# Performance work log

Measured on AMD Instinct MI355X. Metric: run time of the kernel, lower is better.

The kernel has to match this reference:

```python
import jax, jax.numpy as jnp
import numpy as np

N = 40000      # nodes (adj.size(0))
ISIZE = 64     # feature dim
K = 24         # kept kNN neighbors per node after d_cut mask
E = N * K      # learner candidate edges
E_ADJ = N * K  # GCN adjacency edges
OMEGA = 0.9
GAMMA = 2.0
D_CUT = 1.5


def setup_inputs() -> dict:
    key = jax.random.key(0)
    k = jax.random.split(key, 8)
    features = jax.random.normal(k[0], (N, ISIZE), jnp.float32)
    sc = 1.0 / np.sqrt(ISIZE)
    W1 = jax.random.normal(k[1], (ISIZE, ISIZE), jnp.float32) * sc
    b1 = jnp.zeros((ISIZE,), jnp.float32)
    W2 = jax.random.normal(k[2], (ISIZE, ISIZE), jnp.float32) * sc
    b2 = jnp.zeros((ISIZE,), jnp.float32)
    adj_row = jax.random.randint(k[3], (E_ADJ,), 0, N, dtype=jnp.int32)
    adj_col = jax.random.randint(k[4], (E_ADJ,), 0, N, dtype=jnp.int32)
    # kNN-style candidate edges: K neighbors per node, no self loops
    i_idx = jnp.repeat(jnp.arange(N, dtype=jnp.int32), K)
    j_idx = (i_idx + jax.random.randint(k[5], (E,), 1, N, dtype=jnp.int32)) % N
    # precomputed distance prior: s_d = 1/exp(gamma*(d/d_cut)^2)
    dist = jax.random.uniform(k[6], (E,), jnp.float32, 0.1, 2.0)
    s_d = jnp.exp(-GAMMA * (dist / D_CUT) ** 2)
    return {"features": features, "W1": W1, "b1": b1, "W2": W2, "b2": b2,
            "s_d": s_d, "adj_row": adj_row, "adj_col": adj_col,
            "i_idx": i_idx, "j_idx": j_idx}


def _gcn(x, W, b, row, col):
    """PyG GCNConv: symmetric norm with self loops, aggregate src=row into dst=col."""
    xw = x @ W
    deg = 1.0 + jax.ops.segment_sum(jnp.ones((row.shape[0],), jnp.float32), col,
                                    num_segments=N)
    dinv = jax.lax.rsqrt(deg)
    msg = (dinv[row] * dinv[col])[:, None] * xw[row]            # [E_ADJ, ISIZE]
    out = jax.ops.segment_sum(msg, col, num_segments=N)
    return out + (dinv * dinv)[:, None] * xw + b                # self-loop + bias


def reference(features, W1, b1, W2, b2, s_d, adj_row, adj_col, i_idx, j_idx):
    # GCN stack (nlayers=2), ReLU between layers
    h = jax.nn.relu(_gcn(features, W1, b1, adj_row, adj_col))
    h = _gcn(h, W2, b2, adj_row, adj_col)
    # F.normalize(h, p=2, dim=-1)
    h = h / jnp.maximum(jnp.linalg.norm(h, axis=-1, keepdims=True), 1e-12)
    # per-edge cosine scores, clamped at 0, blended with distance prior
    s_val = jnp.sum(h[i_idx] * h[j_idx], axis=-1)               # [E]
    s_val = jax.nn.relu(s_val)
    s_val = OMEGA * s_val + (1.0 - OMEGA) * s_d
    # SparseTensor.to_symmetric(reduce='mean'): average with reverse edge if present
    keys = i_idx * N + j_idx                                    # fits int32 (N=4e4)
    rkeys = j_idx * N + i_idx
    order = jnp.argsort(keys)
    sk = keys[order]
    pos = jnp.clip(jnp.searchsorted(sk, rkeys), 0, E - 1)
    found = sk[pos] == rkeys
    rev = order[pos]
    v_sym = jnp.where(found, 0.5 * (s_val + s_val[rev]), s_val)
    # symmetric COO: original edges + reverse copies (zeroed where reverse existed)
    rows_s = jnp.concatenate([i_idx, j_idx])                    # [2E]
    cols_s = jnp.concatenate([j_idx, i_idx])
    vals_s = jnp.concatenate([v_sym, jnp.where(found, 0.0, v_sym)])
    # normalize_adj_symm: D^{-1/2} S D^{-1/2}
    deg = jax.ops.segment_sum(vals_s, rows_s, num_segments=N)
    dinv = jnp.where(deg > 0, jax.lax.rsqrt(jnp.maximum(deg, 1e-12)), 0.0)
    vals_norm = dinv[rows_s] * vals_s * dinv[cols_s]
    return vals_norm, vals_s
```

## Files before the change

### kernel.cpp

```cpp
#include <hip/hip_runtime.h>

#define N_NODES 40000
#define ISIZE   64
#define KNN     24
#define NE      (N_NODES * KNN)
#define OMEGA   0.9f
#define CAP     64
#define NBUCK   80
#define BCAP    16384
#define JBCAP   16384
#define EPT     8

__device__ __forceinline__ float bf2f(unsigned short s) {
    return __uint_as_float(((unsigned)s) << 16);
}
__device__ __forceinline__ unsigned short f2bf(float f) {
    unsigned u = __float_as_uint(f);
    u += 0x7fffu + ((u >> 16) & 1u);
    return (unsigned short)(u >> 16);
}
__device__ __forceinline__ float bflo(unsigned u) { return __uint_as_float(u << 16); }
__device__ __forceinline__ float bfhi(unsigned u) { return __uint_as_float(u & 0xffff0000u); }
__device__ __forceinline__ unsigned pack2(float lo, float hi) {
    return (unsigned)f2bf(lo) | ((unsigned)f2bf(hi) << 16);
}

__global__ void k_mega1(const float* __restrict__ X, const float* __restrict__ W,
                        unsigned short* __restrict__ Y0, unsigned short* __restrict__ Y1,
                        const int* __restrict__ row, const int* __restrict__ col,
                        const int* __restrict__ j_idx,
                        int* __restrict__ bcnt, unsigned* __restrict__ bbuf,
                        unsigned* __restrict__ ovf2, int* __restrict__ ovf2_cnt,
                        int* __restrict__ jbcnt, unsigned* __restrict__ jbbuf,
                        unsigned* __restrict__ jovf, int* __restrict__ jovf_cnt,
                        unsigned char* __restrict__ revb) {
    __shared__ float sW[64 * 64];
    __shared__ float sX[32 * 64];
    const int GB  = N_NODES / 32;
    const int NBA = (NE + 256 * EPT - 1) / (256 * EPT);
    int bx = blockIdx.x;
    int tid = threadIdx.x;
    if (bx < GB) {
        int row0 = bx * 32;
        for (int t = tid; t < 1024; t += 256)
            ((float4*)sW)[t] = ((const float4*)W)[t];
        for (int t = tid; t < 512; t += 256)
            ((float4*)sX)[t] = ((const float4*)(X + row0 * 64))[t];
        __syncthreads();
        int cc = tid & 63;
        int rl = tid >> 6;
        for (int r = rl; r < 32; r += 4) {
            float acc = 0.0f;
#pragma unroll
            for (int kk = 0; kk < 64; kk++) acc += sX[r * 64 + kk] * sW[kk * 64 + cc];
            if (cc < 32) Y0[(row0 + r) * 32 + cc]      = f2bf(acc);
            else         Y1[(row0 + r) * 32 + cc - 32] = f2bf(acc);
        }
    } else if (bx < GB + 2 * NBA) {
        int* lcnt  = (int*)sW;
        int* lbase = lcnt + NBUCK;
        int blk = bx - GB;
        bool adj = blk < NBA;
        if (!adj) blk -= NBA;
        for (int b = tid; b < NBUCK; b += 256) lcnt[b] = 0;
        __syncthreads();
        int e0 = blk * (256 * EPT);
        int myslot[EPT]; int myb[EPT]; unsigned myp[EPT];
        for (int k = 0; k < EPT; k++) {
            int e = e0 + k * 256 + tid;
            if (e < NE) {
                int b; unsigned p;
                if (adj) { int r = row[e], c = col[e]; b = c >> 9; p = ((unsigned)r << 16) | (unsigned)c; }
                else     { int j = j_idx[e];           b = j >> 9; p = ((unsigned)(j & 511) << 20) | (unsigned)e; }
                myb[k] = b; myp[k] = p;
                myslot[k] = atomicAdd(&lcnt[b], 1);
            } else myb[k] = -1;
        }
        __syncthreads();
        int* gcnt = adj ? bcnt : jbcnt;
        for (int b = tid; b < NBUCK; b += 256)
            lbase[b] = (lcnt[b] > 0) ? atomicAdd(&gcnt[b], lcnt[b]) : 0;
        __syncthreads();
        unsigned* gbuf = adj ? bbuf : jbbuf;
        unsigned* govf = adj ? ovf2 : jovf;
        int* gocnt = adj ? ovf2_cnt : jovf_cnt;
        for (int k = 0; k < EPT; k++) {
            if (myb[k] < 0) continue;
            int pos = lbase[myb[k]] + myslot[k];
            if (pos < BCAP) gbuf[myb[k] * BCAP + pos] = myp[k];
            else { int p = atomicAdd(gocnt, 1); govf[p] = myp[k]; }
        }
    } else {
        int e = (bx - GB - 2 * NBA) * 256 + tid;
        int i = e / KNN;
        int j = j_idx[e];
        const uint4* jj4 = (const uint4*)(j_idx + j * KNN);
        int rt = 255;
#pragma unroll
        for (int k = 5; k >= 0; k--) {
            uint4 u = jj4[k];
            if ((int)u.w == i) rt = 4 * k + 3;
            if ((int)u.z == i) rt = 4 * k + 2;
            if ((int)u.y == i) rt = 4 * k + 1;
            if ((int)u.x == i) rt = 4 * k + 0;
        }
        revb[e] = (unsigned char)rt;
    }
}

__global__ void k_scatter3(const unsigned* __restrict__ bbuf, const int* __restrict__ bcnt,
                           int* __restrict__ cnt, unsigned short* __restrict__ ebuf,
                           unsigned* __restrict__ ovf, int* __restrict__ ovf_cnt,
                           const unsigned* __restrict__ ovf2, const int* __restrict__ ovf2_cnt) {
    __shared__ int lcnt2[512];
    int b = blockIdx.x;
    int tid = threadIdx.x;
    if (tid < 512) lcnt2[tid] = 0;
    __syncthreads();
    int n = min(bcnt[b], BCAP);
    for (int idx = tid; idx < n; idx += 1024) {
        unsigned p = bbuf[b * BCAP + idx];
        int c = (int)(p & 0xffffu), r = (int)(p >> 16);
        int slot = atomicAdd(&lcnt2[c & 511], 1);
        if (slot < CAP) ebuf[c * CAP + slot] = (unsigned short)r;
        else { int q = atomicAdd(ovf_cnt, 1); ovf[q] = p; }
    }
    int m = ovf2_cnt[0];
    for (int idx = tid; idx < m; idx += 1024) {
        unsigned p = ovf2[idx];
        int c = (int)(p & 0xffffu), r = (int)(p >> 16);
        if ((c >> 9) != b) continue;
        int slot = atomicAdd(&lcnt2[c & 511], 1);
        if (slot < CAP) ebuf[c * CAP + slot] = (unsigned short)r;
        else { int q = atomicAdd(ovf_cnt, 1); ovf[q] = p; }
    }
    __syncthreads();
    if (tid < 512) {
        int node = b * 512 + tid;
        if (node < N_NODES) cnt[node] = lcnt2[tid];
    }
}

__global__ void k_gemm2(const unsigned short* __restrict__ X, const float* __restrict__ W,
                        unsigned short* __restrict__ Y0, unsigned short* __restrict__ Y1) {
    __shared__ float sW[64 * 64];
    __shared__ float sX[32 * 64];
    int row0 = blockIdx.x * 32;
    for (int t = threadIdx.x; t < 1024; t += 256)
        ((float4*)sW)[t] = ((const float4*)W)[t];
    for (int t = threadIdx.x; t < 512; t += 256) {
        uint2 u = ((const uint2*)(X + row0 * 64))[t];
        ((float4*)sX)[t] = make_float4(bflo(u.x), bfhi(u.x), bflo(u.y), bfhi(u.y));
    }
    __syncthreads();
    int col = threadIdx.x & 63;
    int rl  = threadIdx.x >> 6;
    for (int r = rl; r < 32; r += 4) {
        float acc = 0.0f;
#pragma unroll
        for (int kk = 0; kk < 64; kk++) acc += sX[r * 64 + kk] * sW[kk * 64 + col];
        if (col < 32) Y0[(row0 + r) * 32 + col]      = f2bf(acc);
        else          Y1[(row0 + r) * 32 + col - 32] = f2bf(acc);
    }
}

template<bool RELU, bool NORM>
__global__ void k_aggf4(const uint4* __restrict__ X0q, const uint4* __restrict__ X1q,
                        uint4* __restrict__ outFq,
                        uint4* __restrict__ O0q, uint4* __restrict__ O1q,
                        const int* __restrict__ cnt,
                        const unsigned short* __restrict__ ebuf, const float* __restrict__ bias,
                        const unsigned* __restrict__ ovf, const int* __restrict__ ovf_cnt) {
    int w = (blockIdx.x * 256 + threadIdx.x) >> 6;
    int lane = threadIdx.x & 63;
    int half = lane >> 5, sl = lane & 31;
    int n = w * 2 + half;
    if (n >= N_NODES) return;
    int deg = cnt[n];
    int bucketed = min(deg, CAP);
    int nb0 = min(bucketed, 32);
    int nb1 = bucketed - nb0;

    int   r0v = 0, r1v = 0;
    float d0v = 0.0f, d1v = 0.0f;
    if (sl < nb0) { r0v = (int)ebuf[n * CAP + sl];      d0v = rsqrtf(1.0f + (float)cnt[r0v]); }
    if (sl < nb1) { r1v = (int)ebuf[n * CAP + 32 + sl]; d1v = rsqrtf(1.0f + (float)cnt[r1v]); }

    int g = sl >> 2;
    int f = sl & 3;

    float a[16];
#pragma unroll
    for (int k = 0; k < 16; k++) a[k] = 0.f;

    int np0 = (nb0 + 7) >> 3;
    int np1 = (nb1 + 7) >> 3;

#pragma unroll 4
    for (int d = 0; d < np0; d++) {
        int   q = 8 * d + g;
        int   r = __shfl(r0v, q, 32);
        float c = __shfl(d0v, q, 32);
        uint4 u0 = X0q[r * 4 + f];
        uint4 u1 = X1q[r * 4 + f];
        a[0]  += c * bflo(u0.x); a[1]  += c * bfhi(u0.x);
        a[2]  += c * bflo(u0.y); a[3]  += c * bfhi(u0.y);
        a[4]  += c * bflo(u0.z); a[5]  += c * bfhi(u0.z);
        a[6]  += c * bflo(u0.w); a[7]  += c * bfhi(u0.w);
        a[8]  += c * bflo(u1.x); a[9]  += c * bfhi(u1.x);
        a[10] += c * bflo(u1.y); a[11] += c * bfhi(u1.y);
        a[12] += c * bflo(u1.z); a[13] += c * bfhi(u1.z);
        a[14] += c * bflo(u1.w); a[15] += c * bfhi(u1.w);
    }
#pragma unroll 4
    for (int d = 0; d < np1; d++) {
        int   q = 8 * d + g;
        int   r = __shfl(r1v, q, 32);
        float c = __shfl(d1v, q, 32);
        uint4 u0 = X0q[r * 4 + f];
        uint4 u1 = X1q[r * 4 + f];
        a[0]  += c * bflo(u0.x); a[1]  += c * bfhi(u0.x);
        a[2]  += c * bflo(u0.y); a[3]  += c * bfhi(u0.y);
        a[4]  += c * bflo(u0.z); a[5]  += c * bfhi(u0.z);
        a[6]  += c * bflo(u0.w); a[7]  += c * bfhi(u0.w);
        a[8]  += c * bflo(u1.x); a[9]  += c * bfhi(u1.x);
        a[10] += c * bflo(u1.y); a[11] += c * bfhi(u1.y);
        a[12] += c * bflo(u1.z); a[13] += c * bfhi(u1.z);
        a[14] += c * bflo(u1.w); a[15] += c * bfhi(u1.w);
    }

    if (deg > CAP) {
        int m = ovf_cnt[0];
        for (int k2 = 0; k2 < m; k2++) {
            unsigned p = ovf[k2];
            if ((int)(p & 0xffffu) == n && g == 0) {
                int r = (int)(p >> 16);
                float c = rsqrtf(1.0f + (float)cnt[r]);
                uint4 u0 = X0q[r * 4 + f], u1 = X1q[r * 4 + f];
                a[0]  += c * bflo(u0.x); a[1]  += c * bfhi(u0.x);
                a[2]  += c * bflo(u0.y); a[3]  += c * bfhi(u0.y);
                a[4]  += c * bflo(u0.z); a[5]  += c * bfhi(u0.z);
                a[6]  += c * bflo(u0.w); a[7]  += c * bfhi(u0.w);
                a[8]  += c * bflo(u1.x); a[9]  += c * bfhi(u1.x);
                a[10] += c * bflo(u1.y); a[11] += c * bfhi(u1.y);
                a[12] += c * bflo(u1.z); a[13] += c * bfhi(u1.z);
                a[14] += c * bflo(u1.w); a[15] += c * bfhi(u1.w);
            }
        }
    }

#pragma unroll
    for (int k = 0; k < 16; k++) {
        a[k] += __shfl_xor(a[k], 4, 32);
        a[k] += __shfl_xor(a[k], 8, 32);
        a[k] += __shfl_xor(a[k], 16, 32);
    }

    float di = rsqrtf(1.0f + (float)deg);
    float dd = di * di;
    uint4 s0 = X0q[n * 4 + f], s1 = X1q[n * 4 + f];
    float4 bA0 = ((const float4*)bias)[2 * f];
    float4 bA1 = ((const float4*)bias)[2 * f + 1];
    float4 bB0 = ((const float4*)(bias + 32))[2 * f];
    float4 bB1 = ((const float4*)(bias + 32))[2 * f + 1];
    float v[16];
    v[0]  = di * a[0]  + dd * bflo(s0.x) + bA0.x;
    v[1]  = di * a[1]  + dd * bfhi(s0.x) + bA0.y;
    v[2]  = di * a[2]  + dd * bflo(s0.y) + bA0.z;
    v[3]  = di * a[3]  + dd * bfhi(s0.y) + bA0.w;
    v[4]  = di * a[4]  + dd * bflo(s0.z) + bA1.x;
    v[5]  = di * a[5]  + dd * bfhi(s0.z) + bA1.y;
    v[6]  = di * a[6]  + dd * bflo(s0.w) + bA1.z;
    v[7]  = di * a[7]  + dd * bfhi(s0.w) + bA1.w;
    v[8]  = di * a[8]  + dd * bflo(s1.x) + bB0.x;
    v[9]  = di * a[9]  + dd * bfhi(s1.x) + bB0.y;
    v[10] = di * a[10] + dd * bflo(s1.y) + bB0.z;
    v[11] = di * a[11] + dd * bfhi(s1.y) + bB0.w;
    v[12] = di * a[12] + dd * bflo(s1.z) + bB1.x;
    v[13] = di * a[13] + dd * bfhi(s1.z) + bB1.y;
    v[14] = di * a[14] + dd * bflo(s1.w) + bB1.z;
    v[15] = di * a[15] + dd * bfhi(s1.w) + bB1.w;
    if (RELU) {
#pragma unroll
        for (int k = 0; k < 16; k++) v[k] = fmaxf(v[k], 0.f);
    }
    if (NORM) {
        float s = 0.f;
#pragma unroll
        for (int k = 0; k < 16; k++) s += v[k] * v[k];
        s += __shfl_xor(s, 1, 32);
        s += __shfl_xor(s, 2, 32);
        float inv = 1.0f / fmaxf(sqrtf(s), 1e-12f);
#pragma unroll
        for (int k = 0; k < 16; k++) v[k] *= inv;
        if (g == 0) {
            O0q[n * 4 + f] = make_uint4(pack2(v[0], v[1]),  pack2(v[2], v[3]),
                                        pack2(v[4], v[5]),  pack2(v[6], v[7]));
            O1q[n * 4 + f] = make_uint4(pack2(v[8], v[9]),  pack2(v[10], v[11]),
                                        pack2(v[12], v[13]), pack2(v[14], v[15]));
        }
    } else {
        if (g == 0) {
            outFq[n * 8 + f]     = make_uint4(pack2(v[0], v[1]),  pack2(v[2], v[3]),
                                              pack2(v[4], v[5]),  pack2(v[6], v[7]));
            outFq[n * 8 + 4 + f] = make_uint4(pack2(v[8], v[9]),  pack2(v[10], v[11]),
                                              pack2(v[12], v[13]), pack2(v[14], v[15]));
        }
    }
}

__global__ void k_dotsym(const uint4* __restrict__ H0q, const uint4* __restrict__ H1q,
                         const float* __restrict__ s_d, const int* __restrict__ j_idx,
                         const unsigned char* __restrict__ revb,
                         float* __restrict__ outS) {
    int t = blockIdx.x * 256 + threadIdx.x;
    int e = t >> 3;
    int q = t & 7;
    int g = q >> 2, f = q & 3;
    int i = e / KNN;
    int j = j_idx[e];
    int node = g ? j : i;
    uint4 u0 = H0q[node * 4 + f];
    uint4 u1 = H1q[node * 4 + f];
    uint4 p0, p1;
    p0.x = __shfl_xor(u0.x, 4); p0.y = __shfl_xor(u0.y, 4);
    p0.z = __shfl_xor(u0.z, 4); p0.w = __shfl_xor(u0.w, 4);
    p1.x = __shfl_xor(u1.x, 4); p1.y = __shfl_xor(u1.y, 4);
    p1.z = __shfl_xor(u1.z, 4); p1.w = __shfl_xor(u1.w, 4);
    float s = bflo(u0.x) * bflo(p0.x) + bfhi(u0.x) * bfhi(p0.x)
            + bflo(u0.y) * bflo(p0.y) + bfhi(u0.y) * bfhi(p0.y)
            + bflo(u0.z) * bflo(p0.z) + bfhi(u0.z) * bfhi(p0.z)
            + bflo(u0.w) * bflo(p0.w) + bfhi(u0.w) * bfhi(p0.w)
            + bflo(u1.x) * bflo(p1.x) + bfhi(u1.x) * bfhi(p1.x)
            + bflo(u1.y) * bflo(p1.y) + bfhi(u1.y) * bfhi(p1.y)
            + bflo(u1.z) * bflo(p1.z) + bfhi(u1.z) * bfhi(p1.z)
            + bflo(u1.w) * bflo(p1.w) + bfhi(u1.w) * bfhi(p1.w);
    s += __shfl_xor(s, 1);
    s += __shfl_xor(s, 2);
    if (q == 0) {
        float base = OMEGA * fmaxf(s, 0.0f);
        int rt = revb[e];
        float vv, v2;
        if (rt != 255) {
            int rev = j * KNN + rt;
            vv = base + 0.5f * (1.0f - OMEGA) * (s_d[e] + s_d[rev]);
            v2 = 0.0f;
        } else {
            vv = base + (1.0f - OMEGA) * s_d[e];
            v2 = vv;
        }
        outS[e] = vv;
        outS[NE + e] = v2;
    }
}

__global__ void k_jagg(const unsigned* __restrict__ jbbuf, const int* __restrict__ jbcnt,
                       const float* __restrict__ outS, float* __restrict__ dinv2,
                       const unsigned* __restrict__ jovf, const int* __restrict__ jovf_cnt,
                       const int* __restrict__ j_idx) {
    __shared__ float ld[512];
    int b = blockIdx.x;
    int tid = threadIdx.x;
    if (tid < 512) ld[tid] = 0.0f;
    __syncthreads();
    const float* outSv2 = outS + NE;
    int n = min(jbcnt[b], JBCAP);
    for (int idx = tid; idx < n; idx += 1024) {
        unsigned p = jbbuf[b * JBCAP + idx];
        atomicAdd(&ld[p >> 20], outSv2[p & 0xFFFFFu]);
    }
    int m = jovf_cnt[0];
    for (int t2 = tid; t2 < m; t2 += 1024) {
        int e = (int)(jovf[t2] & 0xFFFFFu);
        int j = j_idx[e];
        if ((j >> 9) == b) atomicAdd(&ld[j & 511], outSv2[e]);
    }
    __syncthreads();
    if (tid < 512) {
        int node = b * 512 + tid;
        if (node < N_NODES) {
            float d = ld[tid];
            const float* pp = outS + node * KNN;
#pragma unroll
            for (int qq = 0; qq < KNN; qq++) d += pp[qq];
            dinv2[node] = (d > 0.0f) ? rsqrtf(fmaxf(d, 1e-12f)) : 0.0f;
        }
    }
}

__global__ void k_norm(const float* __restrict__ outS, const float* __restrict__ dinv2,
                       const int* __restrict__ j_idx, float* __restrict__ out) {
    int t = blockIdx.x * 256 + threadIdx.x;
    int r, c;
    if (t < NE) { r = t / KNN; c = j_idx[t]; }
    else        { int e = t - NE; r = j_idx[e]; c = e / KNN; }
    out[t] = dinv2[r] * outS[t] * dinv2[c];
}

extern "C" void kernel_launch(void* const* d_in, const int* in_sizes, int n_in,
                              void* d_out, int out_size, void* d_ws, size_t ws_size,
                              hipStream_t stream) {
    const float* features = (const float*)d_in[0];
    const float* W1       = (const float*)d_in[1];
    const float* b1       = (const float*)d_in[2];
    const float* W2       = (const float*)d_in[3];
    const float* b2       = (const float*)d_in[4];
    const float* s_d      = (const float*)d_in[5];
    const int*   adj_row  = (const int*)d_in[6];
    const int*   adj_col  = (const int*)d_in[7];
    const int*   j_idx    = (const int*)d_in[9];
    float* out = (float*)d_out;

    const int N64 = N_NODES * 64;
    const int N32 = N_NODES * 32;
    int*   cnt     = (int*)d_ws;
    int*   ovfcnts = cnt + N_NODES;
    int*   bcnt    = ovfcnts + 16;
    int*   jbcnt   = bcnt + NBUCK;
    float* dinv2   = (float*)(jbcnt + NBUCK);
    unsigned short* A0  = (unsigned short*)(dinv2 + N_NODES);
    unsigned short* A1  = A0 + N32;
    unsigned short* B16 = A1 + N32;
    unsigned short* H0  = B16 + N64;
    unsigned short* H1  = H0 + N32;
    unsigned short* ebuf = H1 + N32;
    unsigned* ovf    = (unsigned*)(ebuf + N_NODES * CAP);
    unsigned char* revb = (unsigned char*)(ovf + NE);
    unsigned* bbuf   = (unsigned*)(revb + NE);
    unsigned* jbbuf  = bbuf + NBUCK * BCAP;
    unsigned* ovf2   = jbbuf + NBUCK * JBCAP;
    unsigned* jovf   = ovf2 + NE;

    size_t zero_bytes = (size_t)(N_NODES + 16 + 2 * NBUCK) * 4;
    hipMemsetAsync(cnt, 0, zero_bytes, stream);

    const int GB = N_NODES / 32;
    const int NBA = (NE + 256 * EPT - 1) / (256 * EPT);
    const int RB = NE / 256;
    k_mega1<<<GB + 2 * NBA + RB, 256, 0, stream>>>(
        features, W1, A0, A1, adj_row, adj_col, j_idx,
        bcnt, bbuf, ovf2, ovfcnts + 4, jbcnt, jbbuf, jovf, ovfcnts + 8, revb);

    k_scatter3<<<NBUCK, 1024, 0, stream>>>(bbuf, bcnt, cnt, ebuf,
                                           ovf, ovfcnts, ovf2, ovfcnts + 4);

    k_aggf4<true, false><<<(N_NODES / 2 * 64 + 255) / 256, 256, 0, stream>>>(
        (const uint4*)A0, (const uint4*)A1, (uint4*)B16, nullptr, nullptr,
        cnt, ebuf, b1, ovf, ovfcnts);

    k_gemm2<<<N_NODES / 32, 256, 0, stream>>>(B16, W2, A0, A1);
    k_aggf4<false, true><<<(N_NODES / 2 * 64 + 255) / 256, 256, 0, stream>>>(
        (const uint4*)A0, (const uint4*)A1, nullptr, (uint4*)H0, (uint4*)H1,
        cnt, ebuf, b2, ovf, ovfcnts);

    float* outS = out + 2 * NE;
    k_dotsym<<<NE * 8 / 256, 256, 0, stream>>>(
        (const uint4*)H0, (const uint4*)H1, s_d, j_idx, revb, outS);

    k_jagg<<<NBUCK, 1024, 0, stream>>>(jbbuf, jbcnt, outS, dinv2, jovf, ovfcnts + 8, j_idx);
    k_norm<<<2 * NE / 256, 256, 0, stream>>>(outS, dinv2, j_idx, out);
}
```

Measured before the change: 252.0 us.

## Fuse layer-1 aggregation with second GEMM and halve dot-product threads per edge

Merges the first GCN aggregation (with ReLU and bias) and the following 64x64 GEMM into one 1024-thread kernel. The aggregated rows stay in shared memory and are multiplied by W2 there, which removes the bf16 intermediate round-trip through global memory and one kernel launch. The edge dot-product kernel now uses 4 threads per edge, each loading both endpoints directly instead of exchanging halves through shuffles, so it launches half as many threads. In exchange the fused kernel needs a block-wide barrier and large blocks, with launch bounds forcing one block per SM, which may reduce latency hiding for the gather-heavy aggregation.

Result: faster. 236.4 us (-6.2%).

```diff
diff --git a/kernel.cpp b/kernel.cpp
--- a/kernel.cpp
+++ b/kernel.cpp
@@ -141,41 +141,23 @@
     }
 }
 
-__global__ void k_gemm2(const unsigned short* __restrict__ X, const float* __restrict__ W,
-                        unsigned short* __restrict__ Y0, unsigned short* __restrict__ Y1) {
+__global__ void __launch_bounds__(1024, 1)
+k_aggemm1(const uint4* __restrict__ X0q, const uint4* __restrict__ X1q,
+          const float* __restrict__ W2,
+          unsigned short* __restrict__ C0, unsigned short* __restrict__ C1,
+          const int* __restrict__ cnt,
+          const unsigned short* __restrict__ ebuf, const float* __restrict__ bias,
+          const unsigned* __restrict__ ovf, const int* __restrict__ ovf_cnt) {
     __shared__ float sW[64 * 64];
-    __shared__ float sX[32 * 64];
-    int row0 = blockIdx.x * 32;
-    for (int t = threadIdx.x; t < 1024; t += 256)
-        ((float4*)sW)[t] = ((const float4*)W)[t];
-    for (int t = threadIdx.x; t < 512; t += 256) {
-        uint2 u = ((const uint2*)(X + row0 * 64))[t];
-        ((float4*)sX)[t] = make_float4(bflo(u.x), bfhi(u.x), bflo(u.y), bfhi(u.y));
-    }
-    __syncthreads();
-    int col = threadIdx.x & 63;
-    int rl  = threadIdx.x >> 6;
-    for (int r = rl; r < 32; r += 4) {
-        float acc = 0.0f;
-#pragma unroll
-        for (int kk = 0; kk < 64; kk++) acc += sX[r * 64 + kk] * sW[kk * 64 + col];
-        if (col < 32) Y0[(row0 + r) * 32 + col]      = f2bf(acc);
-        else          Y1[(row0 + r) * 32 + col - 32] = f2bf(acc);
-    }
-}
-
-template<bool RELU, bool NORM>
-__global__ void k_aggf4(const uint4* __restrict__ X0q, const uint4* __restrict__ X1q,
-                        uint4* __restrict__ outFq,
-                        uint4* __restrict__ O0q, uint4* __restrict__ O1q,
-                        const int* __restrict__ cnt,
-                        const unsigned short* __restrict__ ebuf, const float* __restrict__ bias,
-                        const unsigned* __restrict__ ovf, const int* __restrict__ ovf_cnt) {
-    int w = (blockIdx.x * 256 + threadIdx.x) >> 6;
-    int lane = threadIdx.x & 63;
+    __shared__ float sB[32 * 64];
+    int tid  = threadIdx.x;
+    int lane = tid & 63;
     int half = lane >> 5, sl = lane & 31;
-    int n = w * 2 + half;
-    if (n >= N_NODES) return;
+    int nl = (tid >> 6) * 2 + half;
+    int n  = blockIdx.x * 32 + nl;
+
+    ((float4*)sW)[tid] = ((const float4*)W2)[tid];
+
     int deg = cnt[n];
     int bucketed = min(deg, CAP);
     int nb0 = min(bucketed, 32);
@@ -192,7 +174,6 @@
     float a[16];
 #pragma unroll
     for (int k = 0; k < 16; k++) a[k] = 0.f;
-
     int np0 = (nb0 + 7) >> 3;
     int np1 = (nb1 + 7) >> 3;
 
@@ -228,7 +209,6 @@
         a[12] += c * bflo(u1.z); a[13] += c * bfhi(u1.z);
         a[14] += c * bflo(u1.w); a[15] += c * bfhi(u1.w);
     }
-
     if (deg > CAP) {
         int m = ovf_cnt[0];
         for (int k2 = 0; k2 < m; k2++) {
@@ -248,7 +228,142 @@
             }
         }
     }
-
+#pragma unroll
+    for (int k = 0; k < 16; k++) {
+        a[k] += __shfl_xor(a[k], 4, 32);
+        a[k] += __shfl_xor(a[k], 8, 32);
+        a[k] += __shfl_xor(a[k], 16, 32);
+    }
+
+    float di = rsqrtf(1.0f + (float)deg);
+    float dd = di * di;
+    uint4 s0 = X0q[n * 4 + f], s1 = X1q[n * 4 + f];
+    float4 bA0 = ((const float4*)bias)[2 * f];
+    float4 bA1 = ((const float4*)bias)[2 * f + 1];
+    float4 bB0 = ((const float4*)(bias + 32))[2 * f];
+    float4 bB1 = ((const float4*)(bias + 32))[2 * f + 1];
+    if (g == 0) {
+        float* dst = sB + nl * 64 + 8 * f;
+        dst[0] = fmaxf(di * a[0]  + dd * bflo(s0.x) + bA0.x, 0.f);
+        dst[1] = fmaxf(di * a[1]  + dd * bfhi(s0.x) + bA0.y, 0.f);
+        dst[2] = fmaxf(di * a[2]  + dd * bflo(s0.y) + bA0.z, 0.f);
+        dst[3] = fmaxf(di * a[3]  + dd * bfhi(s0.y) + bA0.w, 0.f);
+        dst[4] = fmaxf(di * a[4]  + dd * bflo(s0.z) + bA1.x, 0.f);
+        dst[5] = fmaxf(di * a[5]  + dd * bfhi(s0.z) + bA1.y, 0.f);
+        dst[6] = fmaxf(di * a[6]  + dd * bflo(s0.w) + bA1.z, 0.f);
+        dst[7] = fmaxf(di * a[7]  + dd * bfhi(s0.w) + bA1.w, 0.f);
+        float* dst2 = dst + 32;
+        dst2[0] = fmaxf(di * a[8]  + dd * bflo(s1.x) + bB0.x, 0.f);
+        dst2[1] = fmaxf(di * a[9]  + dd * bfhi(s1.x) + bB0.y, 0.f);
+        dst2[2] = fmaxf(di * a[10] + dd * bflo(s1.y) + bB0.z, 0.f);
+        dst2[3] = fmaxf(di * a[11] + dd * bfhi(s1.y) + bB0.w, 0.f);
+        dst2[4] = fmaxf(di * a[12] + dd * bflo(s1.z) + bB1.x, 0.f);
+        dst2[5] = fmaxf(di * a[13] + dd * bfhi(s1.z) + bB1.y, 0.f);
+        dst2[6] = fmaxf(di * a[14] + dd * bflo(s1.w) + bB1.z, 0.f);
+        dst2[7] = fmaxf(di * a[15] + dd * bfhi(s1.w) + bB1.w, 0.f);
+    }
+    __syncthreads();
+
+    int col = tid & 63;
+    int r0  = tid >> 6;
+    float acc0 = 0.f, acc1 = 0.f;
+#pragma unroll
+    for (int kk = 0; kk < 64; kk++) {
+        float wv = sW[kk * 64 + col];
+        acc0 += sB[r0 * 64 + kk] * wv;
+        acc1 += sB[(r0 + 16) * 64 + kk] * wv;
+    }
+    int na = blockIdx.x * 32 + r0;
+    int nb = na + 16;
+    if (col < 32) {
+        C0[na * 32 + col] = f2bf(acc0);
+        C0[nb * 32 + col] = f2bf(acc1);
+    } else {
+        C1[na * 32 + col - 32] = f2bf(acc0);
+        C1[nb * 32 + col - 32] = f2bf(acc1);
+    }
+}
+
+__global__ void k_aggf4(const uint4* __restrict__ X0q, const uint4* __restrict__ X1q,
+                        uint4* __restrict__ O0q, uint4* __restrict__ O1q,
+                        const int* __restrict__ cnt,
+                        const unsigned short* __restrict__ ebuf, const float* __restrict__ bias,
+                        const unsigned* __restrict__ ovf, const int* __restrict__ ovf_cnt) {
+    int w = (blockIdx.x * 256 + threadIdx.x) >> 6;
+    int lane = threadIdx.x & 63;
+    int half = lane >> 5, sl = lane & 31;
+    int n = w * 2 + half;
+    if (n >= N_NODES) return;
+    int deg = cnt[n];
+    int bucketed = min(deg, CAP);
+    int nb0 = min(bucketed, 32);
+    int nb1 = bucketed - nb0;
+
+    int   r0v = 0, r1v = 0;
+    float d0v = 0.0f, d1v = 0.0f;
+    if (sl < nb0) { r0v = (int)ebuf[n * CAP + sl];      d0v = rsqrtf(1.0f + (float)cnt[r0v]); }
+    if (sl < nb1) { r1v = (int)ebuf[n * CAP + 32 + sl]; d1v = rsqrtf(1.0f + (float)cnt[r1v]); }
+
+    int g = sl >> 2;
+    int f = sl & 3;
+
+    float a[16];
+#pragma unroll
+    for (int k = 0; k < 16; k++) a[k] = 0.f;
+    int np0 = (nb0 + 7) >> 3;
+    int np1 = (nb1 + 7) >> 3;
+
+#pragma unroll 4
+    for (int d = 0; d < np0; d++) {
+        int   q = 8 * d + g;
+        int   r = __shfl(r0v, q, 32);
+        float c = __shfl(d0v, q, 32);
+        uint4 u0 = X0q[r * 4 + f];
+        uint4 u1 = X1q[r * 4 + f];
+        a[0]  += c * bflo(u0.x); a[1]  += c * bfhi(u0.x);
+        a[2]  += c * bflo(u0.y); a[3]  += c * bfhi(u0.y);
+        a[4]  += c * bflo(u0.z); a[5]  += c * bfhi(u0.z);
+        a[6]  += c * bflo(u0.w); a[7]  += c * bfhi(u0.w);
+        a[8]  += c * bflo(u1.x); a[9]  += c * bfhi(u1.x);
+        a[10] += c * bflo(u1.y); a[11] += c * bfhi(u1.y);
+        a[12] += c * bflo(u1.z); a[13] += c * bfhi(u1.z);
+        a[14] += c * bflo(u1.w); a[15] += c * bfhi(u1.w);
+    }
+#pragma unroll 4
+    for (int d = 0; d < np1; d++) {
+        int   q = 8 * d + g;
+        int   r = __shfl(r1v, q, 32);
+        float c = __shfl(d1v, q, 32);
+        uint4 u0 = X0q[r * 4 + f];
+        uint4 u1 = X1q[r * 4 + f];
+        a[0]  += c * bflo(u0.x); a[1]  += c * bfhi(u0.x);
+        a[2]  += c * bflo(u0.y); a[3]  += c * bfhi(u0.y);
+        a[4]  += c * bflo(u0.z); a[5]  += c * bfhi(u0.z);
+        a[6]  += c * bflo(u0.w); a[7]  += c * bfhi(u0.w);
+        a[8]  += c * bflo(u1.x); a[9]  += c * bfhi(u1.x);
+        a[10] += c * bflo(u1.y); a[11] += c * bfhi(u1.y);
+        a[12] += c * bflo(u1.z); a[13] += c * bfhi(u1.z);
+        a[14] += c * bflo(u1.w); a[15] += c * bfhi(u1.w);
+    }
+    if (deg > CAP) {
+        int m = ovf_cnt[0];
+        for (int k2 = 0; k2 < m; k2++) {
+            unsigned p = ovf[k2];
+            if ((int)(p & 0xffffu) == n && g == 0) {
+                int r = (int)(p >> 16);
+                float c = rsqrtf(1.0f + (float)cnt[r]);
+                uint4 u0 = X0q[r * 4 + f], u1 = X1q[r * 4 + f];
+                a[0]  += c * bflo(u0.x); a[1]  += c * bfhi(u0.x);
+                a[2]  += c * bflo(u0.y); a[3]  += c * bfhi(u0.y);
+                a[4]  += c * bflo(u0.z); a[5]  += c * bfhi(u0.z);
+                a[6]  += c * bflo(u0.w); a[7]  += c * bfhi(u0.w);
+                a[8]  += c * bflo(u1.x); a[9]  += c * bfhi(u1.x);
+                a[10] += c * bflo(u1.y); a[11] += c * bfhi(u1.y);
+                a[12] += c * bflo(u1.z); a[13] += c * bfhi(u1.z);
+                a[14] += c * bflo(u1.w); a[15] += c * bfhi(u1.w);
+            }
+        }
+    }
 #pragma unroll
     for (int k = 0; k < 16; k++) {
         a[k] += __shfl_xor(a[k], 4, 32);
@@ -280,32 +395,20 @@
     v[13] = di * a[13] + dd * bfhi(s1.z) + bB1.y;
     v[14] = di * a[14] + dd * bflo(s1.w) + bB1.z;
     v[15] = di * a[15] + dd * bfhi(s1.w) + bB1.w;
-    if (RELU) {
-#pragma unroll
-        for (int k = 0; k < 16; k++) v[k] = fmaxf(v[k], 0.f);
-    }
-    if (NORM) {
-        float s = 0.f;
-#pragma unroll
-        for (int k = 0; k < 16; k++) s += v[k] * v[k];
-        s += __shfl_xor(s, 1, 32);
-        s += __shfl_xor(s, 2, 32);
-        float inv = 1.0f / fmaxf(sqrtf(s), 1e-12f);
-#pragma unroll
-        for (int k = 0; k < 16; k++) v[k] *= inv;
-        if (g == 0) {
-            O0q[n * 4 + f] = make_uint4(pack2(v[0], v[1]),  pack2(v[2], v[3]),
-                                        pack2(v[4], v[5]),  pack2(v[6], v[7]));
-            O1q[n * 4 + f] = make_uint4(pack2(v[8], v[9]),  pack2(v[10], v[11]),
-                                        pack2(v[12], v[13]), pack2(v[14], v[15]));
-        }
-    } else {
-        if (g == 0) {
-            outFq[n * 8 + f]     = make_uint4(pack2(v[0], v[1]),  pack2(v[2], v[3]),
-                                              pack2(v[4], v[5]),  pack2(v[6], v[7]));
-            outFq[n * 8 + 4 + f] = make_uint4(pack2(v[8], v[9]),  pack2(v[10], v[11]),
-                                              pack2(v[12], v[13]), pack2(v[14], v[15]));
-        }
+
+    float s = 0.f;
+#pragma unroll
+    for (int k = 0; k < 16; k++) s += v[k] * v[k];
+    s += __shfl_xor(s, 1, 32);
+    s += __shfl_xor(s, 2, 32);
+    float inv = 1.0f / fmaxf(sqrtf(s), 1e-12f);
+#pragma unroll
+    for (int k = 0; k < 16; k++) v[k] *= inv;
+    if (g == 0) {
+        O0q[n * 4 + f] = make_uint4(pack2(v[0], v[1]),  pack2(v[2], v[3]),
+                                    pack2(v[4], v[5]),  pack2(v[6], v[7]));
+        O1q[n * 4 + f] = make_uint4(pack2(v[8], v[9]),  pack2(v[10], v[11]),
+                                    pack2(v[12], v[13]), pack2(v[14], v[15]));
     }
 }
 
@@ -314,30 +417,25 @@
                          const unsigned char* __restrict__ revb,
                          float* __restrict__ outS) {
     int t = blockIdx.x * 256 + threadIdx.x;
-    int e = t >> 3;
-    int q = t & 7;
-    int g = q >> 2, f = q & 3;
+    int e = t >> 2;
+    int f = t & 3;
     int i = e / KNN;
     int j = j_idx[e];
-    int node = g ? j : i;
-    uint4 u0 = H0q[node * 4 + f];
-    uint4 u1 = H1q[node * 4 + f];
-    uint4 p0, p1;
-    p0.x = __shfl_xor(u0.x, 4); p0.y = __shfl_xor(u0.y, 4);
-    p0.z = __shfl_xor(u0.z, 4); p0.w = __shfl_xor(u0.w, 4);
-    p1.x = __shfl_xor(u1.x, 4); p1.y = __shfl_xor(u1.y, 4);
-    p1.z = __shfl_xor(u1.z, 4); p1.w = __shfl_xor(u1.w, 4);
-    float s = bflo(u0.x) * bflo(p0.x) + bfhi(u0.x) * bfhi(p0.x)
-            + bflo(u0.y) * bflo(p0.y) + bfhi(u0.y) * bfhi(p0.y)
-            + bflo(u0.z) * bflo(p0.z) + bfhi(u0.z) * bfhi(p0.z)
-            + bflo(u0.w) * bflo(p0.w) + bfhi(u0.w) * bfhi(p0.w)
-            + bflo(u1.x) * bflo(p1.x) + bfhi(u1.x) * bfhi(p1.x)
-            + bflo(u1.y) * bflo(p1.y) + bfhi(u1.y) * bfhi(p1.y)
-            + bflo(u1.z) * bflo(p1.z) + bfhi(u1.z) * bfhi(p1.z)
-            + bflo(u1.w) * bflo(p1.w) + bfhi(u1.w) * bfhi(p1.w);
+    uint4 a0 = H0q[i * 4 + f];
+    uint4 b0 = H0q[j * 4 + f];
+    uint4 a1 = H1q[i * 4 + f];
+    uint4 b1 = H1q[j * 4 + f];
+    float s = bflo(a0.x) * bflo(b0.x) + bfhi(a0.x) * bfhi(b0.x)
+            + bflo(a0.y) * bflo(b0.y) + bfhi(a0.y) * bfhi(b0.y)
+            + bflo(a0.z) * bflo(b0.z) + bfhi(a0.z) * bfhi(b0.z)
+            + bflo(a0.w) * bflo(b0.w) + bfhi(a0.w) * bfhi(b0.w)
+            + bflo(a1.x) * bflo(b1.x) + bfhi(a1.x) * bfhi(b1.x)
+            + bflo(a1.y) * bflo(b1.y) + bfhi(a1.y) * bfhi(b1.y)
+            + bflo(a1.z) * bflo(b1.z) + bfhi(a1.z) * bfhi(b1.z)
+            + bflo(a1.w) * bflo(b1.w) + bfhi(a1.w) * bfhi(b1.w);
     s += __shfl_xor(s, 1);
     s += __shfl_xor(s, 2);
-    if (q == 0) {
+    if (f == 0) {
         float base = OMEGA * fmaxf(s, 0.0f);
         int rt = revb[e];
         float vv, v2;
@@ -411,7 +509,6 @@
     const int*   j_idx    = (const int*)d_in[9];
     float* out = (float*)d_out;
 
-    const int N64 = N_NODES * 64;
     const int N32 = N_NODES * 32;
     int*   cnt     = (int*)d_ws;
     int*   ovfcnts = cnt + N_NODES;
@@ -420,8 +517,9 @@
     float* dinv2   = (float*)(jbcnt + NBUCK);
     unsigned short* A0  = (unsigned short*)(dinv2 + N_NODES);
     unsigned short* A1  = A0 + N32;
-    unsigned short* B16 = A1 + N32;
-    unsigned short* H0  = B16 + N64;
+    unsigned short* C0  = A1 + N32;
+    unsigned short* C1  = C0 + N32;
+    unsigned short* H0  = C1 + N32;
     unsigned short* H1  = H0 + N32;
     unsigned short* ebuf = H1 + N32;
     unsigned* ovf    = (unsigned*)(ebuf + N_NODES * CAP);
@@ -444,17 +542,16 @@
     k_scatter3<<<NBUCK, 1024, 0, stream>>>(bbuf, bcnt, cnt, ebuf,
                                            ovf, ovfcnts, ovf2, ovfcnts + 4);
 
-    k_aggf4<true, false><<<(N_NODES / 2 * 64 + 255) / 256, 256, 0, stream>>>(
-        (const uint4*)A0, (const uint4*)A1, (uint4*)B16, nullptr, nullptr,
+    k_aggemm1<<<N_NODES / 32, 1024, 0, stream>>>(
+        (const uint4*)A0, (const uint4*)A1, W2, C0, C1,
         cnt, ebuf, b1, ovf, ovfcnts);
 
-    k_gemm2<<<N_NODES / 32, 256, 0, stream>>>(B16, W2, A0, A1);
-    k_aggf4<false, true><<<(N_NODES / 2 * 64 + 255) / 256, 256, 0, stream>>>(
-        (const uint4*)A0, (const uint4*)A1, nullptr, (uint4*)H0, (uint4*)H1,
+    k_aggf4<<<(N_NODES / 2 * 64 + 255) / 256, 256, 0, stream>>>(
+        (const uint4*)C0, (const uint4*)C1, (uint4*)H0, (uint4*)H1,
         cnt, ebuf, b2, ovf, ovfcnts);
 
     float* outS = out + 2 * NE;
-    k_dotsym<<<NE * 8 / 256, 256, 0, stream>>>(
+    k_dotsym<<<NE * 4 / 256, 256, 0, stream>>>(
         (const uint4*)H0, (const uint4*)H1, s_d, j_idx, revb, outS);
 
     k_jagg<<<NBUCK, 1024, 0, stream>>>(jbbuf, jbcnt, outS, dinv2, jovf, ovfcnts + 8, j_idx);
```
